# Performance work log

Measured on AMD Instinct MI355X. Metric: run time of the kernel, lower is better.

## Reference

```python
import jax, jax.numpy as jnp
import numpy as np

D = 768
B, T = 4, 4096


def _layernorm(x, gamma, bias):
    # Faithful to the (buggy) original: (x - mu/sqrt(var)) * gamma + bias,
    # with torch's default unbiased variance (ddof=1).
    mu = jnp.mean(x, axis=-1, keepdims=True)
    var = jnp.var(x, axis=-1, keepdims=True, ddof=1)
    return (x - mu / jnp.sqrt(var)) * gamma + bias


def setup_inputs() -> dict:
    key = jax.random.key(0)
    ks = jax.random.split(key, 8)
    # kaiming_uniform_ default: bound = sqrt(6 / fan_in) with a=sqrt(5) -> gain = sqrt(2/(1+5)) = sqrt(1/3)
    # bound = gain * sqrt(3/fan_in) = sqrt(1/fan_in)
    bound_attn = 1.0 / np.sqrt(D)
    bound_lin = 1.0 / np.sqrt(D)  # torch Linear default init bound
    return {
        "x": jax.random.normal(ks[0], (B, T, D), dtype=jnp.float32),
        "ln1_g": jnp.ones((D,), jnp.float32),
        "ln1_b": jnp.zeros((D,), jnp.float32),
        "wq": jax.random.uniform(ks[1], (D, D), jnp.float32, -bound_attn, bound_attn),
        "wk": jax.random.uniform(ks[2], (D, D), jnp.float32, -bound_attn, bound_attn),
        "wv": jax.random.uniform(ks[3], (D, D), jnp.float32, -bound_attn, bound_attn),
        "ln2_g": jnp.ones((D,), jnp.float32),
        "ln2_b": jnp.zeros((D,), jnp.float32),
        "fc1_w": jax.random.uniform(ks[4], (D, D), jnp.float32, -bound_lin, bound_lin),
        "fc1_b": jax.random.uniform(ks[5], (D,), jnp.float32, -bound_lin, bound_lin),
        "fc2_w": jax.random.uniform(ks[6], (D, D), jnp.float32, -bound_lin, bound_lin),
        "fc2_b": jax.random.uniform(ks[7], (D,), jnp.float32, -bound_lin, bound_lin),
    }


def reference(x, ln1_g, ln1_b, wq, wk, wv, ln2_g, ln2_b, fc1_w, fc1_b, fc2_w, fc2_b):
    d_model = x.shape[-1]
    # LN 1
    y = _layernorm(x, ln1_g, ln1_b)
    # Naive single-head attention (no causal mask, scale 1/sqrt(d_model))
    q = jnp.einsum("btk,kd->btd", y, wq)
    k = jnp.einsum("btk,kd->btd", y, wk)
    v = jnp.einsum("btk,kd->btd", y, wv)
    scale = 1.0 / jnp.sqrt(jnp.asarray(d_model, y.dtype))
    a = jax.nn.softmax(jnp.einsum("bqd,bkd->bqk", q, k) * scale, axis=-1)
    y = jnp.einsum("bqt,btd->bqd", a, v)
    # LN 2
    y = _layernorm(y, ln2_g, ln2_b)
    # MLP: Linear -> ReLU -> Linear (Dropout in eval mode = identity)
    h = jax.nn.relu(jnp.einsum("btd,od->bto", y, fc1_w) + fc1_b)
    y = jnp.einsum("btd,od->bto", h, fc2_w) + fc2_b
    # Residual
    return x + y
```

## Files before the change

kernel.cpp:

```cpp
#include <hip/hip_runtime.h>
#include <hip/hip_bf16.h>


#define DDIM 768
#define TT   4096
#define NB   4
#define ROWS (NB * TT)

using bf16 = __hip_bfloat16;
typedef __bf16 bf16x8 __attribute__((ext_vector_type(8)));
typedef float  f32x4  __attribute__((ext_vector_type(4)));

__device__ __forceinline__ float to_f(float x) { return x; }
__device__ __forceinline__ float to_f(bf16 x) { return __bfloat162float(x); }

__device__ __forceinline__ void gload16(const void* g, void* l) {
#if __has_builtin(__builtin_amdgcn_global_load_lds)
  __builtin_amdgcn_global_load_lds(
      (const __attribute__((address_space(1))) void*)g,
      (__attribute__((address_space(3))) void*)l, 16, 0, 0);
#else
  int lane = threadIdx.x & 63;
  ((int4*)l)[lane] = *(const int4*)g;
#endif
}

template <int MODE, int NT, int MT>
__global__ __launch_bounds__(256) void gemm_bt(
    const bf16* __restrict__ A, int lda, long sA,
    const bf16* __restrict__ B, int ldb, long sB,
    void* __restrict__ Cout, int ldc, long sC, int K, float scale,
    const float* __restrict__ bias, const float* __restrict__ resid,
    float* __restrict__ Lsum) {
  __shared__ __align__(16) bf16 As[128 * 32];
  __shared__ __align__(16) bf16 Bs[128 * 32];
  __shared__ float Lred[128];

  int bx, by, bz;
  if constexpr (NT > 0) {
    const int h   = blockIdx.x;
    const int xcd = h & 7;
    const int s   = h >> 3;
    bx = s % NT;
    const int group = (s / NT) * 8 + xcd;
    by = group % MT;
    bz = group / MT;
  } else {
    bx = blockIdx.x; by = blockIdx.y; bz = blockIdx.z;
  }

  A += (long)bz * sA;
  B += (long)bz * sB;

  const int tid  = threadIdx.x;
  const int wave = tid >> 6;
  const int lane = tid & 63;
  const int l16  = lane & 15;
  const int lq   = lane >> 4;
  const int wm   = wave >> 1;
  const int wn   = wave & 1;
  const long tileM = (long)by * 128;
  const long tileN = (long)bx * 128;

  if constexpr (MODE == 5) {
    if (tid < 128) Lred[tid] = 0.f;
  }

  f32x4 acc[4][4] = {};

  const int c0 = wave * 128 + lane;
  const int c1 = c0 + 64;
  bf16* ldsA0 = &As[(wave * 128 + 0) * 8];
  bf16* ldsA1 = &As[(wave * 128 + 64) * 8];
  bf16* ldsB0 = &Bs[(wave * 128 + 0) * 8];
  bf16* ldsB1 = &Bs[(wave * 128 + 64) * 8];
  const long ar0 = (tileM + (c0 >> 2)) * (long)lda + (c0 & 3) * 8;
  const long ar1 = (tileM + (c1 >> 2)) * (long)lda + (c1 & 3) * 8;
  const long br0 = (tileN + (c0 >> 2)) * (long)ldb + (c0 & 3) * 8;
  const long br1 = (tileN + (c1 >> 2)) * (long)ldb + (c1 & 3) * 8;

  for (int k0 = 0; k0 < K; k0 += 32) {
    gload16(A + ar0 + k0, ldsA0);
    gload16(A + ar1 + k0, ldsA1);
    gload16(B + br0 + k0, ldsB0);
    gload16(B + br1 + k0, ldsB1);
    __syncthreads();

    bf16x8 af[4], bf_[4];
#pragma unroll
    for (int i = 0; i < 4; ++i)
      af[i] = *(const bf16x8*)&As[(wm * 64 + i * 16 + l16) * 32 + lq * 8];
#pragma unroll
    for (int j = 0; j < 4; ++j)
      bf_[j] = *(const bf16x8*)&Bs[(wn * 64 + j * 16 + l16) * 32 + lq * 8];
#pragma unroll
    for (int i = 0; i < 4; ++i)
#pragma unroll
      for (int j = 0; j < 4; ++j)
        acc[i][j] = __builtin_amdgcn_mfma_f32_16x16x32_bf16(af[i], bf_[j],
                                                            acc[i][j], 0, 0, 0);
    __syncthreads();
  }

  char* Cz = (char*)Cout;
  const long base_m = tileM + wm * 64;
  const long base_n = tileN + wn * 64;

  if constexpr (MODE == 5) {
    float ps[4][4] = {};
#pragma unroll
    for (int i = 0; i < 4; ++i)
#pragma unroll
      for (int j = 0; j < 4; ++j)
#pragma unroll
        for (int r = 0; r < 4; ++r) {
          const long row = base_m + i * 16 + lq * 4 + r;
          const long col = base_n + j * 16 + l16;
          float p = __expf(acc[i][j][r] * scale);
          ((bf16*)Cz)[(long)bz * sC + row * ldc + col] = __float2bfloat16(p);
          ps[i][r] += p;
        }
#pragma unroll
    for (int i = 0; i < 4; ++i)
#pragma unroll
      for (int r = 0; r < 4; ++r) {
        float v = ps[i][r];
        v += __shfl_xor(v, 1);
        v += __shfl_xor(v, 2);
        v += __shfl_xor(v, 4);
        v += __shfl_xor(v, 8);
        if (l16 == 0)
          atomicAdd(&Lred[wm * 64 + i * 16 + lq * 4 + r], v);
      }
    __syncthreads();
    if (tid < 128) atomicAdd(&Lsum[(long)bz * TT + tileM + tid], Lred[tid]);
  } else if constexpr (MODE == 6) {
#pragma unroll
    for (int i = 0; i < 4; ++i)
#pragma unroll
      for (int r = 0; r < 4; ++r) {
        const long row = base_m + i * 16 + lq * 4 + r;
        const float inv = 1.0f / Lsum[(long)bz * TT + row];
#pragma unroll
        for (int j = 0; j < 4; ++j) {
          const long col = base_n + j * 16 + l16;
          ((bf16*)Cz)[(long)bz * sC + row * ldc + col] =
              __float2bfloat16(acc[i][j][r] * inv);
        }
      }
  } else {
#pragma unroll
    for (int i = 0; i < 4; ++i)
#pragma unroll
      for (int j = 0; j < 4; ++j)
#pragma unroll
        for (int r = 0; r < 4; ++r) {
          const long row = base_m + i * 16 + lq * 4 + r;
          const long col = base_n + j * 16 + l16;
          float v = acc[i][j][r];
          if constexpr (MODE == 3) {
            v += bias[col];
            v = v > 0.f ? v : 0.f;
            ((bf16*)Cz)[(long)bz * sC + row * ldc + col] = __float2bfloat16(v);
          } else {
            v += bias[col] + resid[row * ldc + col];
            ((float*)Cz)[(long)bz * sC + row * ldc + col] = v;
          }
        }
  }
}

__global__ __launch_bounds__(256) void gemm_qkv(
    const bf16* __restrict__ A,
    const bf16* __restrict__ Wq, const bf16* __restrict__ Wk,
    const bf16* __restrict__ Wv, bf16* __restrict__ Qm,
    bf16* __restrict__ Km, bf16* __restrict__ Vt) {
  __shared__ __align__(16) bf16 As[128 * 32];
  __shared__ __align__(16) bf16 Bs[128 * 32];

  const int z = blockIdx.z;
  const bf16* B = (z == 0) ? Wq : (z == 1) ? Wk : Wv;

  const int tid  = threadIdx.x;
  const int wave = tid >> 6;
  const int lane = tid & 63;
  const int l16  = lane & 15;
  const int lq   = lane >> 4;
  const int wm   = wave >> 1;
  const int wn   = wave & 1;
  const long tileM = (long)blockIdx.y * 128;
  const long tileN = (long)blockIdx.x * 128;

  f32x4 acc[4][4] = {};

  const int c0 = wave * 128 + lane;
  const int c1 = c0 + 64;
  bf16* ldsA0 = &As[(wave * 128 + 0) * 8];
  bf16* ldsA1 = &As[(wave * 128 + 64) * 8];
  bf16* ldsB0 = &Bs[(wave * 128 + 0) * 8];
  bf16* ldsB1 = &Bs[(wave * 128 + 64) * 8];
  const long ar0 = (tileM + (c0 >> 2)) * (long)DDIM + (c0 & 3) * 8;
  const long ar1 = (tileM + (c1 >> 2)) * (long)DDIM + (c1 & 3) * 8;
  const long br0 = (tileN + (c0 >> 2)) * (long)DDIM + (c0 & 3) * 8;
  const long br1 = (tileN + (c1 >> 2)) * (long)DDIM + (c1 & 3) * 8;

  for (int k0 = 0; k0 < DDIM; k0 += 32) {
    gload16(A + ar0 + k0, ldsA0);
    gload16(A + ar1 + k0, ldsA1);
    gload16(B + br0 + k0, ldsB0);
    gload16(B + br1 + k0, ldsB1);
    __syncthreads();

    bf16x8 af[4], bf_[4];
#pragma unroll
    for (int i = 0; i < 4; ++i)
      af[i] = *(const bf16x8*)&As[(wm * 64 + i * 16 + l16) * 32 + lq * 8];
#pragma unroll
    for (int j = 0; j < 4; ++j)
      bf_[j] = *(const bf16x8*)&Bs[(wn * 64 + j * 16 + l16) * 32 + lq * 8];
#pragma unroll
    for (int i = 0; i < 4; ++i)
#pragma unroll
      for (int j = 0; j < 4; ++j)
        acc[i][j] = __builtin_amdgcn_mfma_f32_16x16x32_bf16(af[i], bf_[j],
                                                            acc[i][j], 0, 0, 0);
    __syncthreads();
  }

  const long base_m = tileM + wm * 64;
  const long base_n = tileN + wn * 64;
  bf16* Cp = (z == 0) ? Qm : (z == 1) ? Km : Vt;
#pragma unroll
  for (int i = 0; i < 4; ++i) {
#pragma unroll
    for (int j = 0; j < 4; ++j) {
#pragma unroll
      for (int r = 0; r < 4; ++r) {
        const long row = base_m + i * 16 + lq * 4 + r;
        const long col = base_n + j * 16 + l16;
        float v = acc[i][j][r];
        if (z < 2)
          Cp[row * DDIM + col] = __float2bfloat16(v);
        else
          Cp[col * (long)ROWS + row] = __float2bfloat16(v);
      }
    }
  }
}

template <typename T>
__global__ __launch_bounds__(256) void ln_kernel(
    const T* __restrict__ in, const float* __restrict__ g,
    const float* __restrict__ beta, bf16* __restrict__ out,
    float* __restrict__ Lzero) {
  const long row = blockIdx.x;
  if (Lzero != nullptr && threadIdx.x == 0) Lzero[row] = 0.f;
  const T* xr = in + row * DDIM;
  const int t = threadIdx.x;
  float v0 = to_f(xr[t]), v1 = to_f(xr[t + 256]), v2 = to_f(xr[t + 512]);
  float s = v0 + v1 + v2;
  float q = v0 * v0 + v1 * v1 + v2 * v2;
#pragma unroll
  for (int o = 32; o; o >>= 1) {
    s += __shfl_down(s, o);
    q += __shfl_down(q, o);
  }
  __shared__ float sb[4], qb[4];
  if ((t & 63) == 0) { sb[t >> 6] = s; qb[t >> 6] = q; }
  __syncthreads();
  const float S = sb[0] + sb[1] + sb[2] + sb[3];
  const float Q = qb[0] + qb[1] + qb[2] + qb[3];
  const float mu  = S * (1.0f / 768.0f);
  const float var = (Q - 768.0f * mu * mu) * (1.0f / 767.0f);
  const float sub = mu / sqrtf(var);
  bf16* orow = out + row * DDIM;
  orow[t]       = __float2bfloat16((v0 - sub) * g[t]       + beta[t]);
  orow[t + 256] = __float2bfloat16((v1 - sub) * g[t + 256] + beta[t + 256]);
  orow[t + 512] = __float2bfloat16((v2 - sub) * g[t + 512] + beta[t + 512]);
}

__global__ void prep_weights(const float* __restrict__ wq,
                             const float* __restrict__ wk,
                             const float* __restrict__ wv,
                             const float* __restrict__ f1,
                             const float* __restrict__ f2,
                             bf16* wqt, bf16* wkt, bf16* wvt, bf16* f1b,
                             bf16* f2b) {
  __shared__ float tile[32][33];
  const float* src;
  bf16* dst;
  bool tr = true;
  switch (blockIdx.z) {
    case 0: src = wq; dst = wqt; break;
    case 1: src = wk; dst = wkt; break;
    case 2: src = wv; dst = wvt; break;
    case 3: src = f1; dst = f1b; tr = false; break;
    default: src = f2; dst = f2b; tr = false; break;
  }
  const int tx = threadIdx.x, ty = threadIdx.y;
  const int x = blockIdx.x * 32 + tx;
  const int y = blockIdx.y * 32 + ty;
  if (tr) {
#pragma unroll
    for (int r = 0; r < 4; ++r) tile[ty + 8 * r][tx] = src[(y + 8 * r) * DDIM + x];
    __syncthreads();
    const int ox = blockIdx.y * 32 + tx;
    const int oy = blockIdx.x * 32 + ty;
#pragma unroll
    for (int r = 0; r < 4; ++r)
      dst[(oy + 8 * r) * DDIM + ox] = __float2bfloat16(tile[tx][ty + 8 * r]);
  } else {
#pragma unroll
    for (int r = 0; r < 4; ++r)
      dst[(y + 8 * r) * DDIM + x] = __float2bfloat16(src[(y + 8 * r) * DDIM + x]);
  }
}

extern "C" void kernel_launch(void* const* d_in, const int* in_sizes, int n_in,
                              void* d_out, int out_size, void* d_ws,
                              size_t ws_size, hipStream_t stream) {
  const float* x     = (const float*)d_in[0];
  const float* ln1_g = (const float*)d_in[1];
  const float* ln1_b = (const float*)d_in[2];
  const float* wq    = (const float*)d_in[3];
  const float* wk    = (const float*)d_in[4];
  const float* wv    = (const float*)d_in[5];
  const float* ln2_g = (const float*)d_in[6];
  const float* ln2_b = (const float*)d_in[7];
  const float* f1w   = (const float*)d_in[8];
  const float* f1bias= (const float*)d_in[9];
  const float* f2w   = (const float*)d_in[10];
  const float* f2bias= (const float*)d_in[11];
  float* out = (float*)d_out;

  char* ws = (char*)d_ws;
  size_t off = 0;
  auto take = [&](size_t bytes) -> char* {
    char* p = ws + off;
    off += (bytes + 255) & ~(size_t)255;
    return p;
  };
  const size_t WB = (size_t)DDIM * DDIM * sizeof(bf16);
  const size_t MB = (size_t)ROWS * DDIM * sizeof(bf16);
  bf16* wqt = (bf16*)take(WB);
  bf16* wkt = (bf16*)take(WB);
  bf16* wvt = (bf16*)take(WB);
  bf16* f1b = (bf16*)take(WB);
  bf16* f2b = (bf16*)take(WB);
  float* Lsum = (float*)take((size_t)ROWS * sizeof(float));
  bf16* y1  = (bf16*)take(MB);
  bf16* Qm  = (bf16*)take(MB);
  bf16* Km  = (bf16*)take(MB);
  bf16* Vt  = (bf16*)take(MB);
  bf16* Sb  = (bf16*)take((size_t)NB * TT * TT * sizeof(bf16));
  bf16* O  = y1;
  bf16* y2 = Qm;
  bf16* h  = Km;

  prep_weights<<<dim3(24, 24, 5), dim3(32, 8), 0, stream>>>(
      wq, wk, wv, f1w, f2w, wqt, wkt, wvt, f1b, f2b);

  ln_kernel<float><<<ROWS, 256, 0, stream>>>(x, ln1_g, ln1_b, y1, Lsum);

  gemm_qkv<<<dim3(6, 128, 3), 256, 0, stream>>>(y1, wqt, wkt, wvt, Qm, Km, Vt);

  const float scale = 0.03608439182435161f;
  gemm_bt<5, 32, 32><<<dim3(32 * 32 * NB), 256, 0, stream>>>(
      Qm, DDIM, (long)TT * DDIM, Km, DDIM, (long)TT * DDIM, Sb, TT,
      (long)TT * TT, DDIM, scale, nullptr, nullptr, Lsum);

  gemm_bt<6, 6, 32><<<dim3(6 * 32 * NB), 256, 0, stream>>>(
      Sb, TT, (long)TT * TT, Vt, ROWS, (long)TT, O, DDIM, (long)TT * DDIM, TT,
      1.f, nullptr, nullptr, Lsum);

  ln_kernel<bf16><<<ROWS, 256, 0, stream>>>(O, ln2_g, ln2_b, y2, nullptr);

  gemm_bt<3, 0, 0><<<dim3(6, 128, 1), 256, 0, stream>>>(
      y2, DDIM, 0, f1b, DDIM, 0, h, DDIM, 0, DDIM, 1.f, f1bias, nullptr,
      nullptr);
  gemm_bt<4, 0, 0><<<dim3(6, 128, 1), 256, 0, stream>>>(
      h, DDIM, 0, f2b, DDIM, 0, out, DDIM, 0, DDIM, 1.f, f2bias, x, nullptr);
}
```

Baseline: 632.7 us.

## Swap GEMM operand roles so epilogues write contiguous 4-element vectors

New measurement: 660.0 us. +4.3%, slower.

```diff
diff --git a/kernel.cpp b/kernel.cpp
--- a/kernel.cpp
+++ b/kernel.cpp
@@ -10,9 +10,15 @@
 using bf16 = __hip_bfloat16;
 typedef __bf16 bf16x8 __attribute__((ext_vector_type(8)));
 typedef float  f32x4  __attribute__((ext_vector_type(4)));
+typedef unsigned short us4 __attribute__((ext_vector_type(4)));
 
 __device__ __forceinline__ float to_f(float x) { return x; }
 __device__ __forceinline__ float to_f(bf16 x) { return __bfloat162float(x); }
+
+__device__ __forceinline__ unsigned short bfb(float f) {
+  bf16 b = __float2bfloat16(f);
+  return __builtin_bit_cast(unsigned short, b);
+}
 
 __device__ __forceinline__ void gload16(const void* g, void* l) {
 #if __has_builtin(__builtin_amdgcn_global_load_lds)
@@ -25,7 +31,7 @@
 #endif
 }
 
-template <int MODE, int NT, int MT>
+template <int MODE, int SWZ, int NT, int MT>
 __global__ __launch_bounds__(256) void gemm_bt(
     const bf16* __restrict__ A, int lda, long sA,
     const bf16* __restrict__ B, int ldb, long sB,
@@ -37,14 +43,22 @@
   __shared__ float Lred[128];
 
   int bx, by, bz;
-  if constexpr (NT > 0) {
+  if constexpr (SWZ == 1) {
     const int h   = blockIdx.x;
     const int xcd = h & 7;
     const int s   = h >> 3;
     bx = s % NT;
-    const int group = (s / NT) * 8 + xcd;
-    by = group % MT;
-    bz = group / MT;
+    const int g = (s / NT) * 8 + xcd;
+    by = g % MT;
+    bz = g / MT;
+  } else if constexpr (SWZ == 2) {
+    const int h   = blockIdx.x;
+    const int xcd = h & 7;
+    const int s   = h >> 3;
+    by = s % MT;
+    const int g = (s / MT) * 8 + xcd;
+    bx = g % NT;
+    bz = g / NT;
   } else {
     bx = blockIdx.x; by = blockIdx.y; bz = blockIdx.z;
   }
@@ -102,76 +116,93 @@
     __syncthreads();
   }
 
-  char* Cz = (char*)Cout;
   const long base_m = tileM + wm * 64;
   const long base_n = tileN + wn * 64;
 
   if constexpr (MODE == 5) {
-    float ps[4][4] = {};
-#pragma unroll
-    for (int i = 0; i < 4; ++i)
-#pragma unroll
-      for (int j = 0; j < 4; ++j)
-#pragma unroll
-        for (int r = 0; r < 4; ++r) {
-          const long row = base_m + i * 16 + lq * 4 + r;
-          const long col = base_n + j * 16 + l16;
-          float p = __expf(acc[i][j][r] * scale);
-          ((bf16*)Cz)[(long)bz * sC + row * ldc + col] = __float2bfloat16(p);
-          ps[i][r] += p;
-        }
-#pragma unroll
-    for (int i = 0; i < 4; ++i)
-#pragma unroll
-      for (int r = 0; r < 4; ++r) {
-        float v = ps[i][r];
-        v += __shfl_xor(v, 1);
-        v += __shfl_xor(v, 2);
-        v += __shfl_xor(v, 4);
-        v += __shfl_xor(v, 8);
-        if (l16 == 0)
-          atomicAdd(&Lred[wm * 64 + i * 16 + lq * 4 + r], v);
+    bf16* P = (bf16*)Cout + (long)bz * sC;
+    float ps[4] = {0.f, 0.f, 0.f, 0.f};
+#pragma unroll
+    for (int j = 0; j < 4; ++j) {
+      const long colq = base_n + j * 16 + l16;
+#pragma unroll
+      for (int i = 0; i < 4; ++i) {
+        const long krow = base_m + i * 16 + lq * 4;
+        const float p0 = exp2f(acc[i][j][0] * scale);
+        const float p1 = exp2f(acc[i][j][1] * scale);
+        const float p2 = exp2f(acc[i][j][2] * scale);
+        const float p3 = exp2f(acc[i][j][3] * scale);
+        ps[j] += (p0 + p1) + (p2 + p3);
+        us4 w = {bfb(p0), bfb(p1), bfb(p2), bfb(p3)};
+        __builtin_nontemporal_store(w, (us4*)(P + colq * (long)ldc + krow));
       }
-    __syncthreads();
-    if (tid < 128) atomicAdd(&Lsum[(long)bz * TT + tileM + tid], Lred[tid]);
+    }
+#pragma unroll
+    for (int j = 0; j < 4; ++j) {
+      float v = ps[j];
+      v += __shfl_xor(v, 16);
+      v += __shfl_xor(v, 32);
+      if (lq == 0) atomicAdd(&Lred[wn * 64 + j * 16 + l16], v);
+    }
+    __syncthreads();
+    if (tid < 128) atomicAdd(&Lsum[(long)bz * TT + tileN + tid], Lred[tid]);
   } else if constexpr (MODE == 6) {
-#pragma unroll
-    for (int i = 0; i < 4; ++i)
-#pragma unroll
-      for (int r = 0; r < 4; ++r) {
-        const long row = base_m + i * 16 + lq * 4 + r;
-        const float inv = 1.0f / Lsum[(long)bz * TT + row];
-#pragma unroll
-        for (int j = 0; j < 4; ++j) {
-          const long col = base_n + j * 16 + l16;
-          ((bf16*)Cz)[(long)bz * sC + row * ldc + col] =
-              __float2bfloat16(acc[i][j][r] * inv);
-        }
+    bf16* Op = (bf16*)Cout + (long)bz * sC;
+    float inv[4];
+#pragma unroll
+    for (int j = 0; j < 4; ++j)
+      inv[j] = 1.0f / Lsum[(long)bz * TT + base_n + j * 16 + l16];
+#pragma unroll
+    for (int j = 0; j < 4; ++j) {
+      const long colq = base_n + j * 16 + l16;
+#pragma unroll
+      for (int i = 0; i < 4; ++i) {
+        const long drow = base_m + i * 16 + lq * 4;
+        us4 w = {bfb(acc[i][j][0] * inv[j]), bfb(acc[i][j][1] * inv[j]),
+                 bfb(acc[i][j][2] * inv[j]), bfb(acc[i][j][3] * inv[j])};
+        *(us4*)(Op + colq * (long)ldc + drow) = w;
       }
+    }
+  } else if constexpr (MODE == 3) {
+    bf16* Hp = (bf16*)Cout;
+#pragma unroll
+    for (int i = 0; i < 4; ++i) {
+      const long drow = base_m + i * 16 + lq * 4;
+      const f32x4 bv = *(const f32x4*)&bias[drow];
+#pragma unroll
+      for (int j = 0; j < 4; ++j) {
+        const long colt = base_n + j * 16 + l16;
+        float v0 = acc[i][j][0] + bv[0]; v0 = v0 > 0.f ? v0 : 0.f;
+        float v1 = acc[i][j][1] + bv[1]; v1 = v1 > 0.f ? v1 : 0.f;
+        float v2 = acc[i][j][2] + bv[2]; v2 = v2 > 0.f ? v2 : 0.f;
+        float v3 = acc[i][j][3] + bv[3]; v3 = v3 > 0.f ? v3 : 0.f;
+        us4 w = {bfb(v0), bfb(v1), bfb(v2), bfb(v3)};
+        *(us4*)(Hp + colt * (long)ldc + drow) = w;
+      }
+    }
   } else {
-#pragma unroll
-    for (int i = 0; i < 4; ++i)
-#pragma unroll
-      for (int j = 0; j < 4; ++j)
-#pragma unroll
-        for (int r = 0; r < 4; ++r) {
-          const long row = base_m + i * 16 + lq * 4 + r;
-          const long col = base_n + j * 16 + l16;
-          float v = acc[i][j][r];
-          if constexpr (MODE == 3) {
-            v += bias[col];
-            v = v > 0.f ? v : 0.f;
-            ((bf16*)Cz)[(long)bz * sC + row * ldc + col] = __float2bfloat16(v);
-          } else {
-            v += bias[col] + resid[row * ldc + col];
-            ((float*)Cz)[(long)bz * sC + row * ldc + col] = v;
-          }
-        }
+    float* Op = (float*)Cout;
+#pragma unroll
+    for (int i = 0; i < 4; ++i) {
+      const long drow = base_m + i * 16 + lq * 4;
+      const f32x4 bv = *(const f32x4*)&bias[drow];
+#pragma unroll
+      for (int j = 0; j < 4; ++j) {
+        const long off = (base_n + j * 16 + l16) * (long)ldc + drow;
+        const f32x4 rs = *(const f32x4*)&resid[off];
+        f32x4 o;
+        o[0] = acc[i][j][0] + bv[0] + rs[0];
+        o[1] = acc[i][j][1] + bv[1] + rs[1];
+        o[2] = acc[i][j][2] + bv[2] + rs[2];
+        o[3] = acc[i][j][3] + bv[3] + rs[3];
+        __builtin_nontemporal_store(o, (f32x4*)(Op + off));
+      }
+    }
   }
 }
 
 __global__ __launch_bounds__(256) void gemm_qkv(
-    const bf16* __restrict__ A,
+    const bf16* __restrict__ Y,
     const bf16* __restrict__ Wq, const bf16* __restrict__ Wk,
     const bf16* __restrict__ Wv, bf16* __restrict__ Qm,
     bf16* __restrict__ Km, bf16* __restrict__ Vt) {
@@ -179,7 +210,8 @@
   __shared__ __align__(16) bf16 Bs[128 * 32];
 
   const int z = blockIdx.z;
-  const bf16* B = (z == 0) ? Wq : (z == 1) ? Wk : Wv;
+  const bf16* Ap = (z == 2) ? Wv : Y;
+  const bf16* Bp = (z == 0) ? Wq : (z == 1) ? Wk : Y;
 
   const int tid  = threadIdx.x;
   const int wave = tid >> 6;
@@ -188,8 +220,8 @@
   const int lq   = lane >> 4;
   const int wm   = wave >> 1;
   const int wn   = wave & 1;
-  const long tileM = (long)blockIdx.y * 128;
-  const long tileN = (long)blockIdx.x * 128;
+  const long tileM = (z == 2) ? (long)blockIdx.x * 128 : (long)blockIdx.y * 128;
+  const long tileN = (z == 2) ? (long)blockIdx.y * 128 : (long)blockIdx.x * 128;
 
   f32x4 acc[4][4] = {};
 
@@ -205,10 +237,10 @@
   const long br1 = (tileN + (c1 >> 2)) * (long)DDIM + (c1 & 3) * 8;
 
   for (int k0 = 0; k0 < DDIM; k0 += 32) {
-    gload16(A + ar0 + k0, ldsA0);
-    gload16(A + ar1 + k0, ldsA1);
-    gload16(B + br0 + k0, ldsB0);
-    gload16(B + br1 + k0, ldsB1);
+    gload16(Ap + ar0 + k0, ldsA0);
+    gload16(Ap + ar1 + k0, ldsA1);
+    gload16(Bp + br0 + k0, ldsB0);
+    gload16(Bp + br1 + k0, ldsB1);
     __syncthreads();
 
     bf16x8 af[4], bf_[4];
@@ -230,22 +262,17 @@
   const long base_m = tileM + wm * 64;
   const long base_n = tileN + wn * 64;
   bf16* Cp = (z == 0) ? Qm : (z == 1) ? Km : Vt;
-#pragma unroll
-  for (int i = 0; i < 4; ++i) {
-#pragma unroll
-    for (int j = 0; j < 4; ++j) {
+  const long ldo = (z < 2) ? (long)DDIM : (long)ROWS;
+#pragma unroll
+  for (int i = 0; i < 4; ++i)
+#pragma unroll
+    for (int j = 0; j < 4; ++j)
 #pragma unroll
       for (int r = 0; r < 4; ++r) {
         const long row = base_m + i * 16 + lq * 4 + r;
         const long col = base_n + j * 16 + l16;
-        float v = acc[i][j][r];
-        if (z < 2)
-          Cp[row * DDIM + col] = __float2bfloat16(v);
-        else
-          Cp[col * (long)ROWS + row] = __float2bfloat16(v);
+        Cp[row * ldo + col] = __float2bfloat16(acc[i][j][r]);
       }
-    }
-  }
 }
 
 template <typename T>
@@ -364,20 +391,20 @@
 
   gemm_qkv<<<dim3(6, 128, 3), 256, 0, stream>>>(y1, wqt, wkt, wvt, Qm, Km, Vt);
 
-  const float scale = 0.03608439182435161f;
-  gemm_bt<5, 32, 32><<<dim3(32 * 32 * NB), 256, 0, stream>>>(
-      Qm, DDIM, (long)TT * DDIM, Km, DDIM, (long)TT * DDIM, Sb, TT,
-      (long)TT * TT, DDIM, scale, nullptr, nullptr, Lsum);
-
-  gemm_bt<6, 6, 32><<<dim3(6 * 32 * NB), 256, 0, stream>>>(
-      Sb, TT, (long)TT * TT, Vt, ROWS, (long)TT, O, DDIM, (long)TT * DDIM, TT,
+  const float scale2 = 0.03608439182435161f * 1.4426950408889634f;
+  gemm_bt<5, 1, 32, 32><<<dim3(32 * 32 * NB), 256, 0, stream>>>(
+      Km, DDIM, (long)TT * DDIM, Qm, DDIM, (long)TT * DDIM, Sb, TT,
+      (long)TT * TT, DDIM, scale2, nullptr, nullptr, Lsum);
+
+  gemm_bt<6, 2, 32, 6><<<dim3(6 * 32 * NB), 256, 0, stream>>>(
+      Vt, ROWS, (long)TT, Sb, TT, (long)TT * TT, O, DDIM, (long)TT * DDIM, TT,
       1.f, nullptr, nullptr, Lsum);
 
   ln_kernel<bf16><<<ROWS, 256, 0, stream>>>(O, ln2_g, ln2_b, y2, nullptr);
 
-  gemm_bt<3, 0, 0><<<dim3(6, 128, 1), 256, 0, stream>>>(
-      y2, DDIM, 0, f1b, DDIM, 0, h, DDIM, 0, DDIM, 1.f, f1bias, nullptr,
+  gemm_bt<3, 2, 128, 6><<<dim3(128 * 6), 256, 0, stream>>>(
+      f1b, DDIM, 0, y2, DDIM, 0, h, DDIM, 0, DDIM, 1.f, f1bias, nullptr,
       nullptr);
-  gemm_bt<4, 0, 0><<<dim3(6, 128, 1), 256, 0, stream>>>(
-      h, DDIM, 0, f2b, DDIM, 0, out, DDIM, 0, DDIM, 1.f, f2bias, x, nullptr);
-}
+  gemm_bt<4, 2, 128, 6><<<dim3(128 * 6), 256, 0, stream>>>(
+      f2b, DDIM, 0, h, DDIM, 0, out, DDIM, 0, DDIM, 1.f, f2bias, x, nullptr);
+}
```
